# Optimization experiments

Measured on AMD Instinct MI355X. Metric: run time of the kernel, lower is better.

The kernel has to match this reference:

```python
import jax, jax.numpy as jnp
import numpy as np

EMB_DIM = 1024
N_HEADS = 16
HEAD_DIM = EMB_DIM // N_HEADS
WINDOW = 128
B, T = 4, 2048


def setup_inputs() -> dict:
    key = jax.random.key(0)
    k1, k2, k3 = jax.random.split(key, 3)
    x = jax.random.normal(k1, (B, T, EMB_DIM), dtype=jnp.float32)
    # nn.Linear weights: stored as [out, in], applied as x @ W^T
    s1 = 1.0 / np.sqrt(EMB_DIM)
    w_qkv = jax.random.uniform(k2, (3 * EMB_DIM, EMB_DIM), jnp.float32, -s1, s1)
    w_out = jax.random.uniform(k3, (EMB_DIM, EMB_DIM), jnp.float32, -s1, s1)
    return {"x": x, "w_qkv": w_qkv, "w_out": w_out}


def reference(x, w_qkv, w_out):
    Bs, Ts, C = x.shape
    scale = HEAD_DIM ** -0.5
    qkv = x @ w_qkv.T                                   # [B,T,3C]
    qkv = qkv.reshape(Bs, Ts, 3, N_HEADS, HEAD_DIM)
    qkv = jnp.transpose(qkv, (2, 0, 3, 1, 4))           # [3,B,H,T,D]
    q, k, v = qkv[0], qkv[1], qkv[2]
    scores = jnp.einsum('bhtd,bhsd->bhts', q, k) * scale  # [B,H,T,T]
    i = jnp.arange(Ts)[:, None]
    j = jnp.arange(Ts)[None, :]
    # causal AND within sliding window: i - WINDOW <= j <= i
    allowed = (j <= i) & (j >= i - WINDOW)               # [T,T] bool
    scores = jnp.where(allowed[None, None], scores, -jnp.inf)
    attn = jax.nn.softmax(scores, axis=-1)
    out = jnp.einsum('bhts,bhsd->bhtd', attn, v)         # [B,H,T,D]
    out = jnp.transpose(out, (0, 2, 1, 3)).reshape(Bs, Ts, C)
    return out @ w_out.T
```

## Files before the change

kernel.cpp:

```cpp
#include <hip/hip_runtime.h>
#include <hip/hip_bf16.h>
#include <stdint.h>

typedef __attribute__((ext_vector_type(8))) short bf16x8;
typedef __attribute__((ext_vector_type(4))) float f32x4;
typedef __attribute__((ext_vector_type(4))) unsigned short u16x4;

#define B_ 4
#define T_ 2048
#define C_ 1024
#define H_ 16
#define D_ 64

__device__ __forceinline__ unsigned short f2bf(float f) {
  union { float f; uint32_t u; } v; v.f = f;
  uint32_t u = v.u;
  uint32_t r = (u + 0x7FFFu + ((u >> 16) & 1u)) >> 16;
  return (unsigned short)r;
}

__global__ void __launch_bounds__(256) cast_f32_bf16(const float* __restrict__ src,
                                                     unsigned short* __restrict__ dst,
                                                     int n4) {
  int i = blockIdx.x * 256 + threadIdx.x;
  if (i >= n4) return;
  float4 f = ((const float4*)src)[i];
  u16x4 o;
  o[0] = f2bf(f.x); o[1] = f2bf(f.y); o[2] = f2bf(f.z); o[3] = f2bf(f.w);
  ((u16x4*)dst)[i] = o;
}

template <int MODE>
__global__ void __launch_bounds__(256) gemm_bt(const unsigned short* __restrict__ A,
                                               const unsigned short* __restrict__ Bm,
                                               unsigned short* __restrict__ qb,
                                               unsigned short* __restrict__ kb,
                                               unsigned short* __restrict__ vb,
                                               float* __restrict__ fo) {
  __shared__ short As[128 * 32];
  __shared__ short Bs[128 * 32];
  const int tid = threadIdx.x;
  const int bm = blockIdx.y * 128;
  const int bn = blockIdx.x * 128;
  const int wave = tid >> 6;
  const int l = tid & 63;
  const int wm = wave >> 1, wn = wave & 1;
  const int lm = l & 15, lq = l >> 4;
  const int lr = l >> 2;
  const int lc = (l & 3) << 3;

  f32x4 acc[4][4];
#pragma unroll
  for (int i = 0; i < 4; i++)
#pragma unroll
    for (int j = 0; j < 4; j++) acc[i][j] = (f32x4){0.f, 0.f, 0.f, 0.f};

  const unsigned short* gsrc[4];
  short* ldst[4];
#pragma unroll
  for (int i = 0; i < 4; i++) {
    int c = wave * 4 + i;
    if (c < 8) {
      gsrc[i] = A + (size_t)(bm + 16 * c + lr) * 1024 + lc;
      ldst[i] = &As[(16 * c) * 32];
    } else {
      gsrc[i] = Bm + (size_t)(bn + 16 * (c - 8) + lr) * 1024 + lc;
      ldst[i] = &Bs[(16 * (c - 8)) * 32];
    }
  }

  for (int k0 = 0; k0 < 1024; k0 += 32) {
    __syncthreads();
#pragma unroll
    for (int i = 0; i < 4; i++) {
      __builtin_amdgcn_global_load_lds(
          (__attribute__((address_space(1))) void*)(uintptr_t)(const void*)(gsrc[i] + k0),
          (__attribute__((address_space(3))) void*)(ldst[i]),
          16, 0, 0);
    }
    __syncthreads();
    bf16x8 af[4], bfr[4];
#pragma unroll
    for (int i = 0; i < 4; i++)
      af[i] = *(const bf16x8*)&As[(wm * 64 + 16 * i + lm) * 32 + 8 * lq];
#pragma unroll
    for (int j = 0; j < 4; j++)
      bfr[j] = *(const bf16x8*)&Bs[(wn * 64 + 16 * j + lm) * 32 + 8 * lq];
#pragma unroll
    for (int i = 0; i < 4; i++)
#pragma unroll
      for (int j = 0; j < 4; j++)
        acc[i][j] = __builtin_amdgcn_mfma_f32_16x16x32_bf16(af[i], bfr[j], acc[i][j], 0, 0, 0);
  }

#pragma unroll
  for (int i = 0; i < 4; i++) {
#pragma unroll
    for (int j = 0; j < 4; j++) {
#pragma unroll
      for (int r = 0; r < 4; r++) {
        int m = bm + wm * 64 + 16 * i + 4 * lq + r;
        int n = bn + wn * 64 + 16 * j + lm;
        float val = acc[i][j][r];
        if (MODE == 0) {
          int which = n >> 10, rem = n & 1023;
          int h = rem >> 6, d = rem & 63;
          int b = m >> 11, t = m & 2047;
          unsigned short* dst = (which == 0) ? qb : ((which == 1) ? kb : vb);
          dst[(((size_t)(b * 16 + h)) * 2048 + t) * 64 + d] = f2bf(val);
        } else {
          fo[(size_t)m * 1024 + n] = val;
        }
      }
    }
  }
}

__global__ void __launch_bounds__(256) attn_swa(const unsigned short* __restrict__ Qb,
                                               const unsigned short* __restrict__ Kb,
                                               const unsigned short* __restrict__ Vb,
                                               unsigned short* __restrict__ Ob) {
  __shared__ short P[4][16 * 40];
  const int wv = threadIdx.x >> 6;
  const int l = threadIdx.x & 63;
  const int wid = blockIdx.x * 4 + wv;
  const int bh = wid >> 7;
  const int t0 = (wid & 127) << 4;
  const int lm = l & 15, lq = l >> 4;
  const size_t base = (size_t)bh * (T_ * D_);

  bf16x8 aq0 = *(const bf16x8*)(Qb + base + (size_t)(t0 + lm) * 64 + 8 * lq);
  bf16x8 aq1 = *(const bf16x8*)(Qb + base + (size_t)(t0 + lm) * 64 + 32 + 8 * lq);

  float mst[4], lst[4];
  f32x4 Oa[4];
#pragma unroll
  for (int r = 0; r < 4; r++) { mst[r] = -1e30f; lst[r] = 0.f; }
#pragma unroll
  for (int jt = 0; jt < 4; jt++) Oa[jt] = (f32x4){0.f, 0.f, 0.f, 0.f};

  const float cs = 0.125f * 1.44269504f;
  int jstart = t0 - 128; if (jstart < 0) jstart = 0;

  for (int j0 = jstart; j0 < t0 + 16; j0 += 32) {
    f32x4 S[2];
#pragma unroll
    for (int hh = 0; hh < 2; hh++) {
      int kr = j0 + 16 * hh + lm; if (kr > T_ - 1) kr = T_ - 1;
      bf16x8 bk0 = *(const bf16x8*)(Kb + base + (size_t)kr * 64 + 8 * lq);
      bf16x8 bk1 = *(const bf16x8*)(Kb + base + (size_t)kr * 64 + 32 + 8 * lq);
      f32x4 s = (f32x4){0.f, 0.f, 0.f, 0.f};
      s = __builtin_amdgcn_mfma_f32_16x16x32_bf16(aq0, bk0, s, 0, 0, 0);
      s = __builtin_amdgcn_mfma_f32_16x16x32_bf16(aq1, bk1, s, 0, 0, 0);
      S[hh] = s;
    }
    float p0s[4], p1s[4], al[4];
#pragma unroll
    for (int r = 0; r < 4; r++) {
      int t = t0 + 4 * lq + r;
      int ja = j0 + lm, jb = j0 + 16 + lm;
      float s0 = ((ja <= t) && (ja + 128 >= t)) ? S[0][r] * cs : -1e30f;
      float s1 = ((jb <= t) && (jb + 128 >= t)) ? S[1][r] * cs : -1e30f;
      float m2 = fmaxf(s0, s1);
#pragma unroll
      for (int off = 1; off < 16; off <<= 1) m2 = fmaxf(m2, __shfl_xor(m2, off));
      float mn = fmaxf(mst[r], m2);
      float a = __builtin_amdgcn_exp2f(mst[r] - mn);
      float p0 = __builtin_amdgcn_exp2f(s0 - mn);
      float p1 = __builtin_amdgcn_exp2f(s1 - mn);
      float ps = p0 + p1;
#pragma unroll
      for (int off = 1; off < 16; off <<= 1) ps += __shfl_xor(ps, off);
      lst[r] = lst[r] * a + ps;
      mst[r] = mn;
      al[r] = a; p0s[r] = p0; p1s[r] = p1;
    }
#pragma unroll
    for (int jt = 0; jt < 4; jt++)
#pragma unroll
      for (int r = 0; r < 4; r++) Oa[jt][r] *= al[r];
#pragma unroll
    for (int r = 0; r < 4; r++) {
      P[wv][(4 * lq + r) * 40 + lm] = (short)f2bf(p0s[r]);
      P[wv][(4 * lq + r) * 40 + 16 + lm] = (short)f2bf(p1s[r]);
    }
    bf16x8 pa = *(const bf16x8*)&P[wv][lm * 40 + 8 * lq];
#pragma unroll
    for (int jt = 0; jt < 4; jt++) {
      bf16x8 vf;
#pragma unroll
      for (int jj = 0; jj < 8; jj++) {
        int kk = j0 + 8 * lq + jj; if (kk > T_ - 1) kk = T_ - 1;
        vf[jj] = (short)Vb[base + (size_t)kk * 64 + 16 * jt + lm];
      }
      Oa[jt] = __builtin_amdgcn_mfma_f32_16x16x32_bf16(pa, vf, Oa[jt], 0, 0, 0);
    }
  }
  const int b = bh >> 4, h = bh & 15;
#pragma unroll
  for (int r = 0; r < 4; r++) {
    float inv = 1.0f / lst[r];
    int t = t0 + 4 * lq + r;
#pragma unroll
    for (int jt = 0; jt < 4; jt++) {
      int c = h * 64 + 16 * jt + lm;
      Ob[((size_t)(b * T_ + t)) * 1024 + c] = f2bf(Oa[jt][r] * inv);
    }
  }
}

extern "C" void kernel_launch(void* const* d_in, const int* in_sizes, int n_in,
                              void* d_out, int out_size, void* d_ws, size_t ws_size,
                              hipStream_t stream) {
  const float* x = (const float*)d_in[0];
  const float* w_qkv = (const float*)d_in[1];
  const float* w_out = (const float*)d_in[2];
  float* out = (float*)d_out;

  unsigned short* xb = (unsigned short*)d_ws;
  unsigned short* wqkvb = xb + (size_t)8192 * 1024;
  unsigned short* woutb = wqkvb + (size_t)3072 * 1024;
  unsigned short* qb = woutb + (size_t)1024 * 1024;
  unsigned short* kb = qb + (size_t)64 * 2048 * 64;
  unsigned short* vb = kb + (size_t)64 * 2048 * 64;

  cast_f32_bf16<<<8192, 256, 0, stream>>>(x, xb, 8192 * 1024 / 4);
  cast_f32_bf16<<<3072, 256, 0, stream>>>(w_qkv, wqkvb, 3072 * 1024 / 4);
  cast_f32_bf16<<<1024, 256, 0, stream>>>(w_out, woutb, 1024 * 1024 / 4);

  gemm_bt<0><<<dim3(24, 64), 256, 0, stream>>>(xb, wqkvb, qb, kb, vb, nullptr);

  attn_swa<<<2048, 256, 0, stream>>>(qb, kb, vb, xb);

  gemm_bt<1><<<dim3(8, 64), 256, 0, stream>>>(xb, woutb, nullptr, nullptr, nullptr, out);
}
```

Before: 223.3 us.

## Double-buffer GEMM LDS loads, swizzle workgroup order, vectorize QKV epilogue via LDS

The GEMM now uses two LDS buffers so that global-to-LDS loads for the next K step are issued while MFMAs run on the current one, leaving one barrier per iteration instead of two. Workgroup indices are remapped so that consecutive blocks walk down M for a fixed N column, which is meant to improve L2 reuse of weight tiles. The QKV epilogue stages the bf16 results in padded LDS and writes 16-byte vectors to the head-major Q/K/V layout in place of scattered 2-byte stores. The costs are more LDS per block, which can lower occupancy, and an extra barrier plus an LDS round trip in the epilogue.

After: 219.4 us. No clear change (-1.7%).

```diff
diff --git a/kernel.cpp b/kernel.cpp
--- a/kernel.cpp
+++ b/kernel.cpp
@@ -37,11 +37,16 @@
                                                unsigned short* __restrict__ kb,
                                                unsigned short* __restrict__ vb,
                                                float* __restrict__ fo) {
-  __shared__ short As[128 * 32];
-  __shared__ short Bs[128 * 32];
+  __shared__ short lds[16896];
   const int tid = threadIdx.x;
-  const int bm = blockIdx.y * 128;
-  const int bn = blockIdx.x * 128;
+
+  const int nwgx = gridDim.x;
+  int flat = blockIdx.y * nwgx + blockIdx.x;
+  int cpx = (nwgx << 6) >> 3;
+  int swz = (flat & 7) * cpx + (flat >> 3);
+  const int bm = (swz & 63) * 128;
+  const int bn = (swz >> 6) * 128;
+
   const int wave = tid >> 6;
   const int l = tid & 63;
   const int wm = wave >> 1, wn = wave & 1;
@@ -56,63 +61,87 @@
     for (int j = 0; j < 4; j++) acc[i][j] = (f32x4){0.f, 0.f, 0.f, 0.f};
 
   const unsigned short* gsrc[4];
-  short* ldst[4];
+  int ldoff[4];
 #pragma unroll
   for (int i = 0; i < 4; i++) {
     int c = wave * 4 + i;
     if (c < 8) {
       gsrc[i] = A + (size_t)(bm + 16 * c + lr) * 1024 + lc;
-      ldst[i] = &As[(16 * c) * 32];
+      ldoff[i] = (16 * c) * 32;
     } else {
       gsrc[i] = Bm + (size_t)(bn + 16 * (c - 8) + lr) * 1024 + lc;
-      ldst[i] = &Bs[(16 * (c - 8)) * 32];
-    }
-  }
+      ldoff[i] = 8192 + (16 * (c - 8)) * 32;
+    }
+  }
+
+#define STAGE(curb, kk)                                                          \
+  do {                                                                           \
+    _Pragma("unroll")                                                            \
+    for (int i = 0; i < 4; i++) {                                                \
+      __builtin_amdgcn_global_load_lds(                                          \
+          (__attribute__((address_space(1))) void*)(uintptr_t)(const void*)(gsrc[i] + (kk)), \
+          (__attribute__((address_space(3))) void*)(lds + ldoff[i] + (curb) * 4096),         \
+          16, 0, 0);                                                             \
+    }                                                                            \
+  } while (0)
+
+  STAGE(0, 0);
+  int cur = 0;
+  __syncthreads();
 
   for (int k0 = 0; k0 < 1024; k0 += 32) {
-    __syncthreads();
-#pragma unroll
-    for (int i = 0; i < 4; i++) {
-      __builtin_amdgcn_global_load_lds(
-          (__attribute__((address_space(1))) void*)(uintptr_t)(const void*)(gsrc[i] + k0),
-          (__attribute__((address_space(3))) void*)(ldst[i]),
-          16, 0, 0);
-    }
-    __syncthreads();
+    if (k0 + 32 < 1024) STAGE(cur ^ 1, k0 + 32);
     bf16x8 af[4], bfr[4];
 #pragma unroll
     for (int i = 0; i < 4; i++)
-      af[i] = *(const bf16x8*)&As[(wm * 64 + 16 * i + lm) * 32 + 8 * lq];
+      af[i] = *(const bf16x8*)&lds[cur * 4096 + (wm * 64 + 16 * i + lm) * 32 + 8 * lq];
 #pragma unroll
     for (int j = 0; j < 4; j++)
-      bfr[j] = *(const bf16x8*)&Bs[(wn * 64 + 16 * j + lm) * 32 + 8 * lq];
+      bfr[j] = *(const bf16x8*)&lds[8192 + cur * 4096 + (wn * 64 + 16 * j + lm) * 32 + 8 * lq];
 #pragma unroll
     for (int i = 0; i < 4; i++)
 #pragma unroll
       for (int j = 0; j < 4; j++)
         acc[i][j] = __builtin_amdgcn_mfma_f32_16x16x32_bf16(af[i], bfr[j], acc[i][j], 0, 0, 0);
-  }
-
-#pragma unroll
-  for (int i = 0; i < 4; i++) {
-#pragma unroll
-    for (int j = 0; j < 4; j++) {
-#pragma unroll
-      for (int r = 0; r < 4; r++) {
-        int m = bm + wm * 64 + 16 * i + 4 * lq + r;
-        int n = bn + wn * 64 + 16 * j + lm;
-        float val = acc[i][j][r];
-        if (MODE == 0) {
-          int which = n >> 10, rem = n & 1023;
-          int h = rem >> 6, d = rem & 63;
-          int b = m >> 11, t = m & 2047;
-          unsigned short* dst = (which == 0) ? qb : ((which == 1) ? kb : vb);
-          dst[(((size_t)(b * 16 + h)) * 2048 + t) * 64 + d] = f2bf(val);
-        } else {
-          fo[(size_t)m * 1024 + n] = val;
+    __syncthreads();
+    cur ^= 1;
+  }
+#undef STAGE
+
+  if (MODE == 0) {
+#pragma unroll
+    for (int i = 0; i < 4; i++)
+#pragma unroll
+      for (int j = 0; j < 4; j++)
+#pragma unroll
+        for (int r = 0; r < 4; r++)
+          lds[(wm * 64 + 16 * i + 4 * lq + r) * 132 + wn * 64 + 16 * j + lm] =
+              (short)f2bf(acc[i][j][r]);
+    __syncthreads();
+#pragma unroll
+    for (int k = 0; k < 8; k++) {
+      int c = tid + 256 * k;
+      int row = c >> 4;
+      int col = (c & 15) << 3;
+      bf16x8 v = *(const bf16x8*)&lds[row * 132 + col];
+      int m = bm + row, n = bn + col;
+      int which = n >> 10, rem = n & 1023;
+      int h = rem >> 6, d = rem & 63;
+      int b = m >> 11, t = m & 2047;
+      unsigned short* dst = (which == 0) ? qb : ((which == 1) ? kb : vb);
+      *(bf16x8*)&dst[(((size_t)(b * 16 + h)) * 2048 + t) * 64 + d] = v;
+    }
+  } else {
+#pragma unroll
+    for (int i = 0; i < 4; i++)
+#pragma unroll
+      for (int j = 0; j < 4; j++)
+#pragma unroll
+        for (int r = 0; r < 4; r++) {
+          int m = bm + wm * 64 + 16 * i + 4 * lq + r;
+          int n = bn + wn * 64 + 16 * j + lm;
+          fo[(size_t)m * 1024 + n] = acc[i][j][r];
         }
-      }
-    }
   }
 }
 
```
